# Kernel optimization log

Hardware: AMD Instinct MI355X
Metric: run time of the kernel (lower is better)

The kernel has to match this reference:

```python
import jax, jax.numpy as jnp
import numpy as np

B, S, D, H = 2, 2048, 2048, 16
HD = D // H  # 128


def setup_inputs() -> dict:
    key = jax.random.key(0)
    ks = jax.random.split(key, 5)
    scale = 0.02
    return {
        "hidden_states": jax.random.normal(ks[0], (B, S, D), dtype=jnp.float32),
        "Wqkv_w": jax.random.normal(ks[1], (3 * D, D), dtype=jnp.float32) * scale,
        "Wqkv_b": jax.random.normal(ks[2], (3 * D,), dtype=jnp.float32) * scale,
        "out_w": jax.random.normal(ks[3], (D, D), dtype=jnp.float32) * scale,
        "out_b": jax.random.normal(ks[4], (D,), dtype=jnp.float32) * scale,
    }


def reference(hidden_states, Wqkv_w, Wqkv_b, out_w, out_b):
    b, s, d = hidden_states.shape
    # QKV projection (torch Linear: x @ W.T + b)
    qkv = hidden_states @ Wqkv_w.T + Wqkv_b          # [b, s, 3d]
    qkv = qkv.reshape(b, s, 3, H, HD)                 # 'b s (three h d)'
    q, k, v = qkv[:, :, 0], qkv[:, :, 1], qkv[:, :, 2]  # [b, s, h, hd]
    softmax_scale = 1.0 / np.float32(np.sqrt(HD))
    # full quadratic scores, matching the naive baddbmm path
    scores = jnp.einsum('bthd,bshd->bhts', q, k) * softmax_scale  # [b,h,t,s]
    # causal=False (module default), dropout_p=0.0 -> no mask, no dropout
    attn = jax.nn.softmax(scores, axis=-1)
    ctx = jnp.einsum('bhts,bshd->bthd', attn, v)      # [b, t, h, hd]
    ctx = ctx.reshape(b, s, d)
    return ctx @ out_w.T + out_b
```

## Files before the change

kernel.cpp:

```cpp
#include <hip/hip_runtime.h>
#include <cstdint>
#include <cstddef>

#define B_ 2
#define S_ 2048
#define D_ 2048
#define H_ 16
#define HD_ 128
#define NTOK 4096
#define NQKV 6144

typedef unsigned short u16;
typedef __attribute__((ext_vector_type(8))) __bf16 bf16x8;
typedef __attribute__((ext_vector_type(4))) float f32x4;

__device__ __forceinline__ u16 f2bf(float f) {
  uint32_t u = __builtin_bit_cast(uint32_t, f);
  u = (u + 0x7FFFu + ((u >> 16) & 1u)) >> 16;
  return (u16)u;
}

__device__ __forceinline__ void gload_lds16(const void* g, void* l) {
  __builtin_amdgcn_global_load_lds(
      (const __attribute__((address_space(1))) void*)g,
      (__attribute__((address_space(3))) void*)l, 16, 0, 0);
}

__global__ void cvt_f32_bf16(const float* __restrict__ src, u16* __restrict__ dst, int n8) {
  int idx = blockIdx.x * blockDim.x + threadIdx.x;
  int stride = gridDim.x * blockDim.x;
  for (int i = idx; i < n8; i += stride) {
    const float4* s = (const float4*)(src + (size_t)i * 8);
    float4 a = s[0], b = s[1];
    union { u16 u[8]; uint4 v; } o;
    o.u[0] = f2bf(a.x); o.u[1] = f2bf(a.y); o.u[2] = f2bf(a.z); o.u[3] = f2bf(a.w);
    o.u[4] = f2bf(b.x); o.u[5] = f2bf(b.y); o.u[6] = f2bf(b.z); o.u[7] = f2bf(b.w);
    *(uint4*)(dst + (size_t)i * 8) = o.v;
  }
}

__device__ __forceinline__ void gemm_bt_tile(
    const u16* __restrict__ A, const u16* __restrict__ B,
    int lda, int ldb, int K, int m0, int n0,
    u16* As, u16* Bs, f32x4 acc[4][4])
{
  const int tid = threadIdx.x;
  const int lane = tid & 63;
  const int wid = tid >> 6;
  const int wr = wid >> 1, wc = wid & 1;
  const int fr = lane & 15, fq = lane >> 4;

  for (int k0 = 0; k0 < K; k0 += 32) {
    __syncthreads();
#pragma unroll
    for (int i = 0; i < 2; ++i) {
      int cbase = (i * 4 + wid) * 64;
      int c = cbase + lane;
      int r = c >> 2, c8 = (c & 3) * 8;
      gload_lds16(A + (size_t)(m0 + r) * lda + k0 + c8, As + (size_t)cbase * 8);
      gload_lds16(B + (size_t)(n0 + r) * ldb + k0 + c8, Bs + (size_t)cbase * 8);
    }
    __syncthreads();

    bf16x8 a[4], b[4];
#pragma unroll
    for (int m = 0; m < 4; ++m)
      a[m] = *(const bf16x8*)&As[(wr * 64 + m * 16 + fr) * 32 + fq * 8];
#pragma unroll
    for (int n = 0; n < 4; ++n)
      b[n] = *(const bf16x8*)&Bs[(wc * 64 + n * 16 + fr) * 32 + fq * 8];
#pragma unroll
    for (int m = 0; m < 4; ++m)
#pragma unroll
      for (int n = 0; n < 4; ++n)
        acc[m][n] = __builtin_amdgcn_mfma_f32_16x16x32_bf16(a[m], b[n], acc[m][n], 0, 0, 0);
  }
}

__global__ __launch_bounds__(256) void qkv_gemm(
    const u16* __restrict__ hsb, const u16* __restrict__ wb,
    const float* __restrict__ bias,
    u16* __restrict__ qb, u16* __restrict__ kb, u16* __restrict__ vT)
{
  __shared__ alignas(16) u16 As[128 * 32];
  __shared__ alignas(16) u16 Bs[128 * 32];
  f32x4 acc[4][4];
  f32x4 z = {0.f, 0.f, 0.f, 0.f};
#pragma unroll
  for (int m = 0; m < 4; ++m)
#pragma unroll
    for (int n = 0; n < 4; ++n) acc[m][n] = z;

  int m0 = blockIdx.x * 128, n0 = blockIdx.y * 128;
  gemm_bt_tile(hsb, wb, D_, D_, D_, m0, n0, As, Bs, acc);

  const float qscale = 0.08838834764831845f;
  const int lane = threadIdx.x & 63;
  const int wid = threadIdx.x >> 6;
  const int wr = wid >> 1, wc = wid & 1;
  const int fr = lane & 15, fq = lane >> 4;
#pragma unroll
  for (int m = 0; m < 4; ++m)
#pragma unroll
    for (int n = 0; n < 4; ++n) {
      int col = n0 + wc * 64 + n * 16 + fr;
      float bv = bias[col];
      int t = col >> 11;
      int d2 = col & 2047;
      int h = d2 >> 7, hd = d2 & 127;
#pragma unroll
      for (int r = 0; r < 4; ++r) {
        int row = m0 + wr * 64 + m * 16 + fq * 4 + r;
        int bb = row >> 11, s = row & 2047;
        int bh = bb * H_ + h;
        float val = acc[m][n][r] + bv;
        if (t == 0)      qb[((size_t)bh * S_ + s) * HD_ + hd] = f2bf(val * qscale);
        else if (t == 1) kb[((size_t)bh * S_ + s) * HD_ + hd] = f2bf(val);
        else             vT[((size_t)bh * HD_ + hd) * S_ + s] = f2bf(val);
      }
    }
}

__global__ __launch_bounds__(256) void out_gemm(
    const u16* __restrict__ ctx, const u16* __restrict__ wo,
    const float* __restrict__ bias, float* __restrict__ out)
{
  __shared__ alignas(16) u16 As[128 * 32];
  __shared__ alignas(16) u16 Bs[128 * 32];
  f32x4 acc[4][4];
  f32x4 z = {0.f, 0.f, 0.f, 0.f};
#pragma unroll
  for (int m = 0; m < 4; ++m)
#pragma unroll
    for (int n = 0; n < 4; ++n) acc[m][n] = z;

  int m0 = blockIdx.x * 128, n0 = blockIdx.y * 128;
  gemm_bt_tile(ctx, wo, D_, D_, D_, m0, n0, As, Bs, acc);

  const int lane = threadIdx.x & 63;
  const int wid = threadIdx.x >> 6;
  const int wr = wid >> 1, wc = wid & 1;
  const int fr = lane & 15, fq = lane >> 4;
#pragma unroll
  for (int m = 0; m < 4; ++m)
#pragma unroll
    for (int n = 0; n < 4; ++n) {
      int col = n0 + wc * 64 + n * 16 + fr;
      float bv = bias[col];
#pragma unroll
      for (int r = 0; r < 4; ++r) {
        int row = m0 + wr * 64 + m * 16 + fq * 4 + r;
        out[(size_t)row * D_ + col] = acc[m][n][r] + bv;
      }
    }
}

#define STAGEKV(kvv, buf) do { _Pragma("unroll") \
  for (int i = 0; i < 4; ++i) { \
    int lk = i * 256 + tid; int rk = lk >> 4, sk = lk & 15; \
    gload_lds16(Kg + (size_t)((kvv) + rk) * HD_ + ((sk ^ (rk & 7)) << 3), \
                &Kl[buf][i * 2048 + wid * 512]); \
    int rv = lk >> 3, sv = lk & 7; \
    gload_lds16(Vg + (size_t)rv * S_ + (kvv) + ((sv ^ (rv & 7)) << 3), \
                &Vl[buf][i * 2048 + wid * 512]); \
  } } while (0)

__global__ __launch_bounds__(256, 2) void attn(
    const u16* __restrict__ qb, const u16* __restrict__ kb,
    const u16* __restrict__ vT, u16* __restrict__ ctx)
{
  __shared__ alignas(1024) u16 Kl[2][64 * 128];
  __shared__ alignas(1024) u16 Vl[2][128 * 64];
  __shared__ alignas(16) u16 Pl[4][32 * 64];

  const int tid = threadIdx.x, lane = tid & 63, wid = tid >> 6;
  const int fr = lane & 15, fq = lane >> 4;
  const int bh = blockIdx.y;
  const int q0 = blockIdx.x * 128 + wid * 32;
  f32x4 z = {0.f, 0.f, 0.f, 0.f};

  const u16* Kg = kb + (size_t)bh * S_ * HD_;
  const u16* Vg = vT + (size_t)bh * HD_ * S_;

  STAGEKV(0, 0);

  const u16* qbase = qb + ((size_t)bh * S_ + q0) * HD_;
  bf16x8 qa[2][4];
#pragma unroll
  for (int h = 0; h < 2; ++h)
#pragma unroll
    for (int kc = 0; kc < 4; ++kc)
      qa[h][kc] = *(const bf16x8*)(qbase + (size_t)(h * 16 + fr) * HD_ + kc * 32 + fq * 8);

  f32x4 accv[2][8];
#pragma unroll
  for (int h = 0; h < 2; ++h)
#pragma unroll
    for (int n = 0; n < 8; ++n) accv[h][n] = z;
  float m_run[2] = {-1e30f, -1e30f};
  float l_run[2] = {0.f, 0.f};

  __syncthreads();
  int cur = 0;

  for (int kv = 0; kv < S_; kv += 64) {
    if (kv + 64 < S_) STAGEKV(kv + 64, cur ^ 1);

    const u16* Kc = Kl[cur];
    const u16* Vc = Vl[cur];

    f32x4 sc[2][4];
#pragma unroll
    for (int j = 0; j < 4; ++j) {
      f32x4 s0 = z, s1 = z;
#pragma unroll
      for (int kc = 0; kc < 4; ++kc) {
        int row = j * 16 + fr;
        bf16x8 kf = *(const bf16x8*)&Kc[row * 128 + ((kc * 32 + fq * 8) ^ ((row & 7) << 3))];
        s0 = __builtin_amdgcn_mfma_f32_16x16x32_bf16(kf, qa[0][kc], s0, 0, 0, 0);
        s1 = __builtin_amdgcn_mfma_f32_16x16x32_bf16(kf, qa[1][kc], s1, 0, 0, 0);
      }
      sc[0][j] = s0; sc[1][j] = s1;
    }

    float pmax[2];
#pragma unroll
    for (int h = 0; h < 2; ++h) {
      float mx = sc[h][0][0];
#pragma unroll
      for (int j = 0; j < 4; ++j)
#pragma unroll
        for (int r = 0; r < 4; ++r) mx = fmaxf(mx, sc[h][j][r]);
      mx = fmaxf(mx, __shfl_xor(mx, 16));
      mx = fmaxf(mx, __shfl_xor(mx, 32));
      pmax[h] = mx;
    }

    int need = (pmax[0] > m_run[0] + 8.f) || (pmax[1] > m_run[1] + 8.f);
    if (__any(need)) {
#pragma unroll
      for (int h = 0; h < 2; ++h) {
        float mn = fmaxf(m_run[h], pmax[h]);
        float corr = __expf(m_run[h] - mn);
        m_run[h] = mn;
        l_run[h] *= corr;
#pragma unroll
        for (int r = 0; r < 4; ++r) {
          float rc = __shfl(corr, (lane & 48) | (fq * 4 + r));
#pragma unroll
          for (int n = 0; n < 8; ++n) accv[h][n][r] *= rc;
        }
      }
    }

    u16* Pw = Pl[wid];
#pragma unroll
    for (int h = 0; h < 2; ++h) {
      float ls = 0.f;
#pragma unroll
      for (int j = 0; j < 4; ++j) {
        union { u16 u[4]; ushort4 v; } pk;
#pragma unroll
        for (int r = 0; r < 4; ++r) {
          float p = __expf(sc[h][j][r] - m_run[h]);
          ls += p;
          pk.u[r] = f2bf(p);
        }
        int prow = h * 16 + fr;
        *(ushort4*)&Pw[prow * 64 + ((j * 16 + fq * 4) ^ ((fr & 7) << 3))] = pk.v;
      }
      ls += __shfl_xor(ls, 16);
      ls += __shfl_xor(ls, 32);
      l_run[h] += ls;
    }

#pragma unroll
    for (int kc = 0; kc < 2; ++kc) {
      int pcol = (kc * 32 + fq * 8) ^ ((fr & 7) << 3);
      bf16x8 pa0 = *(const bf16x8*)&Pw[fr * 64 + pcol];
      bf16x8 pa1 = *(const bf16x8*)&Pw[(16 + fr) * 64 + pcol];
#pragma unroll
      for (int n = 0; n < 8; ++n) {
        int row = n * 16 + fr;
        bf16x8 vf = *(const bf16x8*)&Vc[row * 64 + ((kc * 32 + fq * 8) ^ ((row & 7) << 3))];
        accv[0][n] = __builtin_amdgcn_mfma_f32_16x16x32_bf16(pa0, vf, accv[0][n], 0, 0, 0);
        accv[1][n] = __builtin_amdgcn_mfma_f32_16x16x32_bf16(pa1, vf, accv[1][n], 0, 0, 0);
      }
    }

    __syncthreads();
    cur ^= 1;
  }

  float inv[2][4];
#pragma unroll
  for (int h = 0; h < 2; ++h)
#pragma unroll
    for (int r = 0; r < 4; ++r) {
      float l = __shfl(l_run[h], (lane & 48) | (fq * 4 + r));
      inv[h][r] = 1.f / l;
    }
  u16* cb = ctx + (((size_t)(bh >> 4)) * S_ + blockIdx.x * 128 + wid * 32) * D_ + (size_t)(bh & 15) * HD_;
#pragma unroll
  for (int h = 0; h < 2; ++h)
#pragma unroll
    for (int n = 0; n < 8; ++n)
#pragma unroll
      for (int r = 0; r < 4; ++r) {
        int q = h * 16 + fq * 4 + r;
        cb[(size_t)q * D_ + n * 16 + fr] = f2bf(accv[h][n][r] * inv[h][r]);
      }
}

extern "C" void kernel_launch(void* const* d_in, const int* in_sizes, int n_in,
                              void* d_out, int out_size, void* d_ws, size_t ws_size,
                              hipStream_t stream) {
  const float* hs   = (const float*)d_in[0];
  const float* wqkv = (const float*)d_in[1];
  const float* bqkv = (const float*)d_in[2];
  const float* wo   = (const float*)d_in[3];
  const float* bo   = (const float*)d_in[4];
  float* out = (float*)d_out;

  char* ws = (char*)d_ws;
  u16* hsb   = (u16*)(ws);
  u16* wqkvb = (u16*)(ws + 16777216);
  u16* wob   = (u16*)(ws + 41943040);
  u16* qb    = (u16*)(ws + 50331648);
  u16* kb    = (u16*)(ws + 67108864);
  u16* vT    = (u16*)(ws + 83886080);
  u16* ctx   = (u16*)(ws + 100663296);

  cvt_f32_bf16<<<2048, 256, 0, stream>>>(hs,   hsb,   (B_ * S_ * D_) / 8);
  cvt_f32_bf16<<<2048, 256, 0, stream>>>(wqkv, wqkvb, (NQKV * D_) / 8);
  cvt_f32_bf16<<<1024, 256, 0, stream>>>(wo,   wob,   (D_ * D_) / 8);

  qkv_gemm<<<dim3(NTOK / 128, NQKV / 128), 256, 0, stream>>>(hsb, wqkvb, bqkv, qb, kb, vT);
  attn<<<dim3(S_ / 128, B_ * H_), 256, 0, stream>>>(qb, kb, vT, ctx);
  out_gemm<<<dim3(NTOK / 128, D_ / 128), 256, 0, stream>>>(ctx, wob, bo, out);
}
```

Measured before the change: 307.1 us.

## Double-buffer LDS tiles in projection GEMMs to overlap loads with MFMA

Splits the GEMM K-loop into staging and compute helpers and uses two LDS buffer pairs, so the next K-slice is loaded asynchronously while MFMAs run on the current one. This halves the barriers per K-step and hides global-to-LDS latency in both the QKV and output projection kernels. In exchange, LDS use per block doubles, which may lower occupancy. The loop assumes K is a multiple of 64.

```diff
diff --git a/kernel.cpp b/kernel.cpp
--- a/kernel.cpp
+++ b/kernel.cpp
@@ -39,41 +39,60 @@
   }
 }
 
+
+__device__ __forceinline__ void stage_tiles(
+    const u16* __restrict__ A, const u16* __restrict__ B,
+    int lda, int ldb, int m0, int n0, int k0, u16* As, u16* Bs)
+{
+  const int tid = threadIdx.x;
+  const int lane = tid & 63, wid = tid >> 6;
+#pragma unroll
+  for (int i = 0; i < 2; ++i) {
+    int cbase = (i * 4 + wid) * 64;
+    int c = cbase + lane;
+    int r = c >> 2, c8 = (c & 3) * 8;
+    gload_lds16(A + (size_t)(m0 + r) * lda + k0 + c8, As + (size_t)cbase * 8);
+    gload_lds16(B + (size_t)(n0 + r) * ldb + k0 + c8, Bs + (size_t)cbase * 8);
+  }
+}
+
+__device__ __forceinline__ void compute_step(
+    const u16* As, const u16* Bs, f32x4 acc[4][4],
+    int wr, int wc, int fr, int fq)
+{
+  bf16x8 a[4], b[4];
+#pragma unroll
+  for (int m = 0; m < 4; ++m)
+    a[m] = *(const bf16x8*)&As[(wr * 64 + m * 16 + fr) * 32 + fq * 8];
+#pragma unroll
+  for (int n = 0; n < 4; ++n)
+    b[n] = *(const bf16x8*)&Bs[(wc * 64 + n * 16 + fr) * 32 + fq * 8];
+#pragma unroll
+  for (int m = 0; m < 4; ++m)
+#pragma unroll
+    for (int n = 0; n < 4; ++n)
+      acc[m][n] = __builtin_amdgcn_mfma_f32_16x16x32_bf16(a[m], b[n], acc[m][n], 0, 0, 0);
+}
+
 __device__ __forceinline__ void gemm_bt_tile(
     const u16* __restrict__ A, const u16* __restrict__ B,
     int lda, int ldb, int K, int m0, int n0,
-    u16* As, u16* Bs, f32x4 acc[4][4])
-{
-  const int tid = threadIdx.x;
-  const int lane = tid & 63;
-  const int wid = tid >> 6;
+    u16* As0, u16* Bs0, u16* As1, u16* Bs1, f32x4 acc[4][4])
+{
+  const int lane = threadIdx.x & 63, wid = threadIdx.x >> 6;
   const int wr = wid >> 1, wc = wid & 1;
   const int fr = lane & 15, fq = lane >> 4;
 
-  for (int k0 = 0; k0 < K; k0 += 32) {
+  stage_tiles(A, B, lda, ldb, m0, n0, 0, As0, Bs0);
+  __syncthreads();
+
+  for (int k0 = 0; k0 < K; k0 += 64) {
+    if (k0 + 32 < K) stage_tiles(A, B, lda, ldb, m0, n0, k0 + 32, As1, Bs1);
+    compute_step(As0, Bs0, acc, wr, wc, fr, fq);
     __syncthreads();
-#pragma unroll
-    for (int i = 0; i < 2; ++i) {
-      int cbase = (i * 4 + wid) * 64;
-      int c = cbase + lane;
-      int r = c >> 2, c8 = (c & 3) * 8;
-      gload_lds16(A + (size_t)(m0 + r) * lda + k0 + c8, As + (size_t)cbase * 8);
-      gload_lds16(B + (size_t)(n0 + r) * ldb + k0 + c8, Bs + (size_t)cbase * 8);
-    }
+    if (k0 + 64 < K) stage_tiles(A, B, lda, ldb, m0, n0, k0 + 64, As0, Bs0);
+    compute_step(As1, Bs1, acc, wr, wc, fr, fq);
     __syncthreads();
-
-    bf16x8 a[4], b[4];
-#pragma unroll
-    for (int m = 0; m < 4; ++m)
-      a[m] = *(const bf16x8*)&As[(wr * 64 + m * 16 + fr) * 32 + fq * 8];
-#pragma unroll
-    for (int n = 0; n < 4; ++n)
-      b[n] = *(const bf16x8*)&Bs[(wc * 64 + n * 16 + fr) * 32 + fq * 8];
-#pragma unroll
-    for (int m = 0; m < 4; ++m)
-#pragma unroll
-      for (int n = 0; n < 4; ++n)
-        acc[m][n] = __builtin_amdgcn_mfma_f32_16x16x32_bf16(a[m], b[n], acc[m][n], 0, 0, 0);
   }
 }
 
@@ -82,8 +101,10 @@
     const float* __restrict__ bias,
     u16* __restrict__ qb, u16* __restrict__ kb, u16* __restrict__ vT)
 {
-  __shared__ alignas(16) u16 As[128 * 32];
-  __shared__ alignas(16) u16 Bs[128 * 32];
+  __shared__ alignas(16) u16 As0[128 * 32];
+  __shared__ alignas(16) u16 Bs0[128 * 32];
+  __shared__ alignas(16) u16 As1[128 * 32];
+  __shared__ alignas(16) u16 Bs1[128 * 32];
   f32x4 acc[4][4];
   f32x4 z = {0.f, 0.f, 0.f, 0.f};
 #pragma unroll
@@ -92,7 +113,7 @@
     for (int n = 0; n < 4; ++n) acc[m][n] = z;
 
   int m0 = blockIdx.x * 128, n0 = blockIdx.y * 128;
-  gemm_bt_tile(hsb, wb, D_, D_, D_, m0, n0, As, Bs, acc);
+  gemm_bt_tile(hsb, wb, D_, D_, D_, m0, n0, As0, Bs0, As1, Bs1, acc);
 
   const float qscale = 0.08838834764831845f;
   const int lane = threadIdx.x & 63;
@@ -125,8 +146,10 @@
     const u16* __restrict__ ctx, const u16* __restrict__ wo,
     const float* __restrict__ bias, float* __restrict__ out)
 {
-  __shared__ alignas(16) u16 As[128 * 32];
-  __shared__ alignas(16) u16 Bs[128 * 32];
+  __shared__ alignas(16) u16 As0[128 * 32];
+  __shared__ alignas(16) u16 Bs0[128 * 32];
+  __shared__ alignas(16) u16 As1[128 * 32];
+  __shared__ alignas(16) u16 Bs1[128 * 32];
   f32x4 acc[4][4];
   f32x4 z = {0.f, 0.f, 0.f, 0.f};
 #pragma unroll
@@ -135,7 +158,7 @@
     for (int n = 0; n < 4; ++n) acc[m][n] = z;
 
   int m0 = blockIdx.x * 128, n0 = blockIdx.y * 128;
-  gemm_bt_tile(ctx, wo, D_, D_, D_, m0, n0, As, Bs, acc);
+  gemm_bt_tile(ctx, wo, D_, D_, D_, m0, n0, As0, Bs0, As1, Bs1, acc);
 
   const int lane = threadIdx.x & 63;
   const int wid = threadIdx.x >> 6;
```

New measurement: 321.0 us. +4.6%, slower.

## Rewrite QKV GEMM with 256x192 tiles, double-buffered direct-to-LDS loads and swizzle

Applied to the files above, without the earlier changes.

Replaces the simple 128x128 QKV GEMM with a 512-thread, 256x192-tile kernel. It double-buffers 64-wide K slices in LDS via global_load_lds, uses an XOR swizzle to avoid bank conflicts, and interleaves loads with MFMA phases using s_setprio and explicit waitcnt/barriers. The goal is to hide global memory latency and raise MFMA utilisation for the largest GEMM. The cost is much higher register and LDS use per block and fragile hand-scheduled synchronisation.

```diff
diff --git a/kernel.cpp b/kernel.cpp
--- a/kernel.cpp
+++ b/kernel.cpp
@@ -39,6 +39,113 @@
   }
 }
 
+
+#define PH_MID() do { asm volatile("s_barrier" ::: "memory"); \
+  asm volatile("s_waitcnt lgkmcnt(0)" ::: "memory"); \
+  __builtin_amdgcn_s_setprio(1); } while (0)
+#define PH_END() do { __builtin_amdgcn_s_setprio(0); \
+  asm volatile("s_barrier" ::: "memory"); } while (0)
+#define PH_END_VM(n) do { __builtin_amdgcn_s_setprio(0); \
+  asm volatile("s_waitcnt vmcnt(" #n ")" ::: "memory"); \
+  asm volatile("s_barrier" ::: "memory"); } while (0)
+
+#define STA(sl,buf,ko) gload_lds16(aSrc + (size_t)(sl)*64*D_ + (ko), aDst + (buf)*16384 + (sl)*4096)
+#define STB(sl,buf,ko) gload_lds16(bSrc + (size_t)(sl)*64*D_ + (ko), bDst + (buf)*12288 + (sl)*4096)
+
+#define LOADB(buf) do { _Pragma("unroll") for (int nf = 0; nf < 3; ++nf) \
+  _Pragma("unroll") for (int kk = 0; kk < 2; ++kk) \
+    breg[nf][kk] = *(const bf16x8*)(sB + (buf)*12288 + (wn*48 + nf*16 + fr)*64 + ((((kk<<2)|fq)^swz)<<3)); } while (0)
+#define LOADA(buf,q) do { _Pragma("unroll") for (int mm = 0; mm < 2; ++mm) \
+  _Pragma("unroll") for (int kk = 0; kk < 2; ++kk) \
+    areg[mm][kk] = *(const bf16x8*)(sA + (buf)*16384 + (wm*128 + ((q)*2+mm)*16 + fr)*64 + ((((kk<<2)|fq)^swz)<<3)); } while (0)
+#define MFMA12(q) do { _Pragma("unroll") for (int mm = 0; mm < 2; ++mm) \
+  _Pragma("unroll") for (int nf = 0; nf < 3; ++nf) \
+  _Pragma("unroll") for (int kk = 0; kk < 2; ++kk) \
+    acc[(q)*2+mm][nf] = __builtin_amdgcn_mfma_f32_16x16x32_bf16(areg[mm][kk], breg[nf][kk], acc[(q)*2+mm][nf], 0, 0, 0); } while (0)
+
+__global__ __launch_bounds__(512, 2) void qkv_gemm(
+    const u16* __restrict__ hsb, const u16* __restrict__ wb,
+    const float* __restrict__ bias,
+    u16* __restrict__ qb, u16* __restrict__ kb, u16* __restrict__ vT)
+{
+  __shared__ alignas(1024) u16 sA[2 * 16384];
+  __shared__ alignas(1024) u16 sB[2 * 12288];
+  const int tid = threadIdx.x;
+  const int lane = tid & 63, wid = tid >> 6;
+  const int wm = wid >> 2, wn = wid & 3;
+  const int fr = lane & 15, fq = lane >> 4;
+  const int swz = fr & 7;
+  const int m0 = blockIdx.x * 256, n0 = blockIdx.y * 192;
+
+  const int r8 = tid >> 3, g8 = (tid & 7) ^ (r8 & 7);
+  const u16* aSrc = hsb + (size_t)(m0 + r8) * D_ + g8 * 8;
+  const u16* bSrc = wb  + (size_t)(n0 + r8) * D_ + g8 * 8;
+  u16* aDst = sA + wid * 512;
+  u16* bDst = sB + wid * 512;
+
+  f32x4 acc[8][3];
+  f32x4 z = {0.f, 0.f, 0.f, 0.f};
+#pragma unroll
+  for (int m = 0; m < 8; ++m)
+#pragma unroll
+    for (int n = 0; n < 3; ++n) acc[m][n] = z;
+
+  bf16x8 breg[3][2], areg[2][2];
+
+  STB(0,0,0); STB(1,0,0); STB(2,0,0); STA(0,0,0); STA(1,0,0); STA(2,0,0); STA(3,0,0);
+  STB(0,1,64); STB(1,1,64); STB(2,1,64); STA(0,1,64); STA(2,1,64);
+  asm volatile("s_waitcnt vmcnt(5)" ::: "memory");
+  asm volatile("s_barrier" ::: "memory");
+
+  const int NI = D_ / 128;
+  for (int j = 0; j < NI - 1; ++j) {
+    const int kS = (2*j + 1) * 64;
+    const int kA = (2*j + 2) * 64;
+    const int kB = (2*j + 3) * 64;
+    LOADB(0); LOADA(0,0); STA(1,1,kS); STA(3,1,kS); PH_MID(); MFMA12(0); PH_END();
+    LOADA(0,1);           STB(0,0,kA); STB(1,0,kA); PH_MID(); MFMA12(1); PH_END();
+    LOADA(0,2);           STB(2,0,kA); STA(0,0,kA); PH_MID(); MFMA12(2); PH_END();
+    LOADA(0,3);           STA(2,0,kA);              PH_MID(); MFMA12(3); PH_END_VM(5);
+    LOADB(1); LOADA(1,0); STA(1,0,kA); STA(3,0,kA); PH_MID(); MFMA12(0); PH_END();
+    LOADA(1,1);           STB(0,1,kB); STB(1,1,kB); PH_MID(); MFMA12(1); PH_END();
+    LOADA(1,2);           STB(2,1,kB); STA(0,1,kB); PH_MID(); MFMA12(2); PH_END();
+    LOADA(1,3);           STA(2,1,kB);              PH_MID(); MFMA12(3); PH_END_VM(5);
+  }
+  {
+    const int kS = (2*NI - 1) * 64;
+    LOADB(0); LOADA(0,0); STA(1,1,kS); STA(3,1,kS); PH_MID(); MFMA12(0); PH_END();
+    LOADA(0,1);                                     PH_MID(); MFMA12(1); PH_END();
+    LOADA(0,2);                                     PH_MID(); MFMA12(2); PH_END();
+    LOADA(0,3);                                     PH_MID(); MFMA12(3); PH_END_VM(0);
+    LOADB(1); LOADA(1,0);                           PH_MID(); MFMA12(0); PH_END();
+    LOADA(1,1);                                     PH_MID(); MFMA12(1); PH_END();
+    LOADA(1,2);                                     PH_MID(); MFMA12(2); PH_END();
+    LOADA(1,3);                                     PH_MID(); MFMA12(3); PH_END();
+  }
+
+  const float qscale = 0.08838834764831845f;
+#pragma unroll
+  for (int mf = 0; mf < 8; ++mf)
+#pragma unroll
+    for (int nf = 0; nf < 3; ++nf) {
+      int col = n0 + wn * 48 + nf * 16 + fr;
+      float bv = bias[col];
+      int t = col >> 11;
+      int d2 = col & 2047;
+      int h = d2 >> 7, hd = d2 & 127;
+#pragma unroll
+      for (int r = 0; r < 4; ++r) {
+        int row = m0 + wm * 128 + mf * 16 + fq * 4 + r;
+        int bb = row >> 11, s = row & 2047;
+        int bh = bb * H_ + h;
+        float val = acc[mf][nf][r] + bv;
+        if (t == 0)      qb[((size_t)bh * S_ + s) * HD_ + hd] = f2bf(val * qscale);
+        else if (t == 1) kb[((size_t)bh * S_ + s) * HD_ + hd] = f2bf(val);
+        else             vT[((size_t)bh * HD_ + hd) * S_ + s] = f2bf(val);
+      }
+    }
+}
+
 __device__ __forceinline__ void gemm_bt_tile(
     const u16* __restrict__ A, const u16* __restrict__ B,
     int lda, int ldb, int K, int m0, int n0,
@@ -77,50 +184,6 @@
   }
 }
 
-__global__ __launch_bounds__(256) void qkv_gemm(
-    const u16* __restrict__ hsb, const u16* __restrict__ wb,
-    const float* __restrict__ bias,
-    u16* __restrict__ qb, u16* __restrict__ kb, u16* __restrict__ vT)
-{
-  __shared__ alignas(16) u16 As[128 * 32];
-  __shared__ alignas(16) u16 Bs[128 * 32];
-  f32x4 acc[4][4];
-  f32x4 z = {0.f, 0.f, 0.f, 0.f};
-#pragma unroll
-  for (int m = 0; m < 4; ++m)
-#pragma unroll
-    for (int n = 0; n < 4; ++n) acc[m][n] = z;
-
-  int m0 = blockIdx.x * 128, n0 = blockIdx.y * 128;
-  gemm_bt_tile(hsb, wb, D_, D_, D_, m0, n0, As, Bs, acc);
-
-  const float qscale = 0.08838834764831845f;
-  const int lane = threadIdx.x & 63;
-  const int wid = threadIdx.x >> 6;
-  const int wr = wid >> 1, wc = wid & 1;
-  const int fr = lane & 15, fq = lane >> 4;
-#pragma unroll
-  for (int m = 0; m < 4; ++m)
-#pragma unroll
-    for (int n = 0; n < 4; ++n) {
-      int col = n0 + wc * 64 + n * 16 + fr;
-      float bv = bias[col];
-      int t = col >> 11;
-      int d2 = col & 2047;
-      int h = d2 >> 7, hd = d2 & 127;
-#pragma unroll
-      for (int r = 0; r < 4; ++r) {
-        int row = m0 + wr * 64 + m * 16 + fq * 4 + r;
-        int bb = row >> 11, s = row & 2047;
-        int bh = bb * H_ + h;
-        float val = acc[m][n][r] + bv;
-        if (t == 0)      qb[((size_t)bh * S_ + s) * HD_ + hd] = f2bf(val * qscale);
-        else if (t == 1) kb[((size_t)bh * S_ + s) * HD_ + hd] = f2bf(val);
-        else             vT[((size_t)bh * HD_ + hd) * S_ + s] = f2bf(val);
-      }
-    }
-}
-
 __global__ __launch_bounds__(256) void out_gemm(
     const u16* __restrict__ ctx, const u16* __restrict__ wo,
     const float* __restrict__ bias, float* __restrict__ out)
@@ -335,7 +398,7 @@
   cvt_f32_bf16<<<2048, 256, 0, stream>>>(wqkv, wqkvb, (NQKV * D_) / 8);
   cvt_f32_bf16<<<1024, 256, 0, stream>>>(wo,   wob,   (D_ * D_) / 8);
 
-  qkv_gemm<<<dim3(NTOK / 128, NQKV / 128), 256, 0, stream>>>(hsb, wqkvb, bqkv, qb, kb, vT);
+  qkv_gemm<<<dim3(NTOK / 256, NQKV / 192), 512, 0, stream>>>(hsb, wqkvb, bqkv, qb, kb, vT);
   attn<<<dim3(S_ / 128, B_ * H_), 256, 0, stream>>>(qb, kb, vT, ctx);
   out_gemm<<<dim3(NTOK / 128, D_ / 128), 256, 0, stream>>>(ctx, wob, bo, out);
 }
```

Result: faster. 300.6 us (-2.1%).
